# Optimization experiments

Measured on AMD Instinct MI355X. Metric: run time of the kernel, lower is better.

The kernel has to match this reference:

```python
import jax, jax.numpy as jnp
import numpy as np

PS = 16          # patch size == conv kernel == stride
EPS = 1e-5       # BatchNorm eps (torch default)


def setup_inputs() -> dict:
    key = jax.random.key(0)
    ks = jax.random.split(key, 12)
    B, Cin, H = 64, 3, 256
    D, Dm = 3, 768                      # private_depth, hidden_dim
    P = (H // PS) ** 2                  # num_patches = 256

    x = jax.random.normal(ks[0], (B, Cin, H, H), jnp.float32)
    # patch-embed conv: weight [O, I, kh, kw], bias [O]
    conv0_w = jax.random.normal(ks[1], (Dm, Cin, PS, PS), jnp.float32) * 0.02
    conv0_b = jax.random.normal(ks[2], (Dm,), jnp.float32) * 0.02
    # depth x (1x1 conv + BN): stacked params
    w1 = jax.random.normal(ks[3], (D, Dm, Dm), jnp.float32) * 0.02   # [O, I]
    b1 = jax.random.normal(ks[4], (D, Dm), jnp.float32) * 0.02
    gamma = jnp.ones((D, Dm), jnp.float32)
    beta = jnp.zeros((D, Dm), jnp.float32)
    # positional embedding [1, P, Dm]
    pos_emb = jax.random.normal(ks[5], (1, P, Dm), jnp.float32)
    # mixer Linear [out, in] + bias
    mixer_w = jax.random.normal(ks[6], (Dm, Dm), jnp.float32) * 0.02
    mixer_b = jax.random.normal(ks[7], (Dm,), jnp.float32) * 0.02
    # per-sample random permutation of the P patches (replaces randperm loop)
    perm = jax.vmap(lambda k: jax.random.permutation(k, P))(
        jax.random.split(ks[8], B)).astype(jnp.int32)

    return {"x": x, "conv0_w": conv0_w, "conv0_b": conv0_b, "w1": w1,
            "b1": b1, "gamma": gamma, "beta": beta, "pos_emb": pos_emb,
            "mixer_w": mixer_w, "mixer_b": mixer_b, "perm": perm}


def reference(x, conv0_w, conv0_b, w1, b1, gamma, beta, pos_emb,
              mixer_w, mixer_b, perm):
    B, Cin, H, W = x.shape
    hp, wp = H // PS, W // PS
    Dm = conv0_w.shape[0]

    # non-overlapping patch conv == reshape + matmul
    # x -> [B, hp*wp, Cin*PS*PS] with (c, kh, kw) flattening matching conv weight
    patches = x.reshape(B, Cin, hp, PS, wp, PS).transpose(0, 2, 4, 1, 3, 5)
    patches = patches.reshape(B, hp * wp, Cin * PS * PS)
    h = jax.nn.relu(patches @ conv0_w.reshape(Dm, -1).T + conv0_b)  # [B, P, Dm]

    # private_depth x (1x1 conv -> BN (batch stats, no running stats) -> ReLU)
    for d in range(w1.shape[0]):
        h = h @ w1[d].T + b1[d]
        mu = h.mean(axis=(0, 1))                      # per-channel over (B, H*W)
        var = ((h - mu) ** 2).mean(axis=(0, 1))       # biased variance
        h = (h - mu) * jax.lax.rsqrt(var + EPS) * gamma[d] + beta[d]
        h = jax.nn.relu(h)

    # pos embedding + mixer (ReLU -> Linear)
    h = h + pos_emb
    h = jax.nn.relu(h) @ mixer_w.T + mixer_b          # [B, P, Dm]

    # per-sample pixel shuffle: shuffled[i, j] = h[i, perm[i, j]]
    out = jnp.take_along_axis(h, perm[:, :, None].astype(jnp.int32), axis=1)
    return out
```

## Files before the change

kernel.cpp:

```cpp
#include <hip/hip_runtime.h>
#include <hip/hip_bf16.h>
#include <stdint.h>

#define M_TOT 16384
#define DM 768
#define BM 256
#define BN 192
#define NKT3 12
#define QOFF (128 * DM)

typedef __attribute__((ext_vector_type(4))) float f32x4;
typedef __attribute__((ext_vector_type(8))) short short8;
typedef __attribute__((ext_vector_type(8))) unsigned short ushort8;
typedef __attribute__((ext_vector_type(4))) unsigned short ushort4v;

__device__ __forceinline__ unsigned short f2bf(float f) {
    union { float f; unsigned u; } v; v.f = f;
    unsigned r = v.u + 0x7fffu + ((v.u >> 16) & 1u);
    return (unsigned short)(r >> 16);
}
__device__ __forceinline__ float bf2f(unsigned short h) {
    union { unsigned u; float f; } v; v.u = ((unsigned)h) << 16;
    return v.f;
}

__device__ __forceinline__ void gload_lds16(const unsigned short* g, unsigned short* l) {
    __builtin_amdgcn_global_load_lds(
        (const __attribute__((address_space(1))) void*)g,
        (__attribute__((address_space(3))) void*)l, 16, 0, 0);
}

__global__ __launch_bounds__(256)
void prepim(const float* __restrict__ cw, const float* __restrict__ w1,
            const float* __restrict__ mw, const int* __restrict__ perm,
            const float* __restrict__ x,
            unsigned short* __restrict__ wA, unsigned short* __restrict__ wD,
            unsigned short* __restrict__ wM, int* __restrict__ invp,
            unsigned short* __restrict__ patches)
{
    int b = blockIdx.x;
    if (b < 12288) {
        int t = b * 256 + threadIdx.x;
        int bp = t / 192;
        int q  = t - bp * 192;
        int c   = q >> 6;
        int kh  = (q >> 2) & 15;
        int kw0 = (q & 3) << 2;
        int bb = bp >> 8, p = bp & 255;
        int ph = p >> 4, pw = p & 15;
        const float* src = x + ((((size_t)bb * 3 + c) * 256 + ph * 16 + kh) * 256 + pw * 16 + kw0);
        f32x4 v = *(const f32x4*)src;
        ushort4v o;
        o.x = f2bf(v.x); o.y = f2bf(v.y); o.z = f2bf(v.z); o.w = f2bf(v.w);
        *(ushort4v*)(patches + (size_t)bp * DM + (q << 2)) = o;
    } else if (b < 12288 + 2880) {
        int i = (b - 12288) * 256 + threadIdx.x;
        const float* src; unsigned short* dst; int off;
        if (i < 147456)              { src = cw; dst = wA; off = i; }
        else if (i < 147456+442368)  { src = w1; dst = wD; off = i - 147456; }
        else                         { src = mw; dst = wM; off = i - 589824; }
        f32x4 v = ((const f32x4*)src)[off];
        ushort4v o;
        o.x = f2bf(v.x); o.y = f2bf(v.y); o.z = f2bf(v.z); o.w = f2bf(v.w);
        ((ushort4v*)dst)[off] = o;
    } else {
        int i = (b - 12288 - 2880) * 256 + threadIdx.x;
        int bb = i >> 8;
        invp[(bb << 8) + perm[i]] = i & 255;
    }
}

#define VM4  asm volatile("s_waitcnt vmcnt(4)" ::: "memory");
#define VM0  asm volatile("s_waitcnt vmcnt(0)" ::: "memory");
#define LGKM0 asm volatile("s_waitcnt lgkmcnt(0)" ::: "memory");
#define BARR asm volatile("s_barrier" ::: "memory");

#define PH(AB, BB, MH, KS, LOADB, PRE, POST)                                     \
  {                                                                              \
    if (LOADB) {                                                                 \
      _Pragma("unroll")                                                          \
      for (int j = 0; j < 3; ++j)                                                \
        breg[j] = *(const short8*)((const char*)Bb + (size_t)(BB) * (BN*64*2) +  \
                  (wc * 48 + j * 16 + frow) * 128 + (((KS) * 64 + fq16) ^ rswz));\
    }                                                                            \
    short8 af[4];                                                                \
    _Pragma("unroll")                                                            \
    for (int i = 0; i < 4; ++i)                                                  \
      af[i] = *(const short8*)((const char*)Aa + (size_t)(AB) * (BM*64*2) +      \
              (wr * 128 + (MH) * 64 + i * 16 + frow) * 128 +                     \
              (((KS) * 64 + fq16) ^ rswz));                                      \
    PRE;                                                                         \
    __builtin_amdgcn_s_setprio(1);                                               \
    _Pragma("unroll")                                                            \
    for (int i = 0; i < 4; ++i)                                                  \
      _Pragma("unroll")                                                          \
      for (int j = 0; j < 3; ++j)                                                \
        acc[(MH) * 4 + i][j] = __builtin_amdgcn_mfma_f32_16x16x32_bf16(          \
            af[i], breg[j], acc[(MH) * 4 + i][j], 0, 0, 0);                      \
    __builtin_amdgcn_s_setprio(0);                                               \
    POST;                                                                        \
    BARR                                                                         \
  }

template<int EPI, int BNA>
__global__ __launch_bounds__(512, 2)
void gemm8p(const unsigned short* __restrict__ A,
            const unsigned short* __restrict__ Bw,
            const float* __restrict__ bias,
            void* __restrict__ outp,
            const int* __restrict__ invp,
            float* __restrict__ bnpart,
            const float* __restrict__ ssA)
{
    __shared__ unsigned short Aa[3][BM * 64];
    __shared__ unsigned short Bb[2][BN * 64];

    const int tid  = threadIdx.x;
    const int w    = tid >> 6;
    const int lane = tid & 63;
    const int wr = w >> 2, wc = w & 3;

    int bid = blockIdx.x;
    int nb  = (bid & 7) * 32 + (bid >> 3);
    const int tileM = nb >> 2, tileN = nb & 3;
    const int m0 = tileM * BM, n0 = tileN * BN;

    const int sRow = lane >> 3;
    const int swzc = ((lane & 7) * 16) ^ ((sRow & 7) << 4);
    const unsigned short* gA0 = A  + (size_t)(m0 + w * 32 + sRow) * DM + (swzc >> 1);
    const unsigned short* gB0 = Bw + (size_t)(n0 + w * 24 + sRow) * DM + (swzc >> 1);

    auto STAGE_A = [&](int buf, int kt) {
        #pragma unroll
        for (int j = 0; j < 4; ++j)
            gload_lds16(gA0 + (size_t)j * 8 * DM + kt * 64,
                        &Aa[buf][(w * 32 + j * 8) * 64]);
    };
    auto STAGE_B = [&](int buf, int kt) {
        #pragma unroll
        for (int j = 0; j < 3; ++j)
            gload_lds16(gB0 + (size_t)j * 8 * DM + kt * 64,
                        &Bb[buf][(w * 24 + j * 8) * 64]);
    };

    const int rRow0 = w * 32 + (lane >> 3);
    const unsigned short* gAr = A + (size_t)(m0 + rRow0) * DM + (lane & 7) * 8;
    const int wrswz = (lane >> 3) << 4;
    ushort8 aldr[4];

    auto ALOAD = [&](int t) {
        #pragma unroll
        for (int j = 0; j < 4; ++j)
            aldr[j] = *(const ushort8*)(gAr + (size_t)j * 8 * DM + t * 64);
    };
    auto XFORM = [&](int t, int tb) {
        const int k0 = t * 64 + (lane & 7) * 8;
        f32x4 sa = *(const f32x4*)(ssA + k0);
        f32x4 sb = *(const f32x4*)(ssA + k0 + 4);
        f32x4 ha = *(const f32x4*)(ssA + DM + k0);
        f32x4 hb = *(const f32x4*)(ssA + DM + k0 + 4);
        #pragma unroll
        for (int j = 0; j < 4; ++j) {
            int row = rRow0 + j * 8;
            ushort8 u = aldr[j];
            ushort8 o;
            #pragma unroll
            for (int e = 0; e < 8; ++e) {
                float f = bf2f(u[e]);
                float sc = (e < 4) ? sa[e] : sb[e - 4];
                float sh = (e < 4) ? ha[e] : hb[e - 4];
                o[e] = f2bf(fmaxf(fmaf(sc, f, sh), 0.0f));
            }
            *(ushort8*)((char*)Aa + (size_t)tb * (BM*64*2) + row * 128 +
                        (((lane & 7) * 16) ^ wrswz)) = o;
        }
    };

    const int frow = lane & 15;
    const int fq16 = (lane >> 4) * 16;
    const int rswz = (lane & 7) << 4;

    f32x4 acc[8][3] = {};
    short8 breg[3];

    if (BNA == 0) {
        STAGE_A(0, 0);
        STAGE_B(0, 0);
        STAGE_A(1, 1);
        VM4
        BARR
    } else {
        ALOAD(0); XFORM(0, 0);
        ALOAD(1); XFORM(1, 1);
        STAGE_B(0, 0);
        VM0
        LGKM0
        BARR
    }

    if (BNA == 0) {
        #pragma unroll
        for (int kt = 0; kt < NKT3; ++kt) {
            const int ab = kt % 3, bb = kt & 1;
            PH(ab, bb, 0, 0, 1, { if (kt < 11) STAGE_B((kt + 1) & 1, kt + 1); }, {})
            PH(ab, bb, 1, 0, 0, { if (kt < 10) STAGE_A((kt + 2) % 3, kt + 2); }, {})
            PH(ab, bb, 0, 1, 1, {}, {})
            if (kt < 10)       { PH(ab, bb, 1, 1, 0, {}, { VM4 }) }
            else if (kt == 10) { PH(ab, bb, 1, 1, 0, {}, { VM0 }) }
            else               { PH(ab, bb, 1, 1, 0, {}, {}) }
        }
    } else {
        #pragma unroll 3
        for (int kt = 0; kt < NKT3; ++kt) {
            const int ab = kt % 3, bb = kt & 1;
            const int ab1 = (ab == 2) ? 0 : ab + 1;
            PH(ab, bb, 0, 0, 1, { if (kt < 11) STAGE_B((kt + 1) & 1, kt + 1); }, {})
            PH(ab, bb, 1, 0, 0, { if (kt >= 1 && kt < 11) XFORM(kt + 1, ab1); },
                                { if (kt >= 1 && kt < 11) LGKM0 })
            PH(ab, bb, 0, 1, 1, {}, {})
            PH(ab, bb, 1, 1, 0, {}, { if (kt < 11) VM0
                                      if (kt < 10) ALOAD(kt + 2); })
        }
    }

    const int crow = (lane >> 4) * 4;
    const int ccol = lane & 15;
    const int nbase = n0 + wc * 48;

    float bv[3];
    #pragma unroll
    for (int j = 0; j < 3; ++j) bv[j] = bias[nbase + j * 16 + ccol];

    if (EPI == 0) {
        unsigned short* O = (unsigned short*)outp;
        #pragma unroll
        for (int mi = 0; mi < 8; ++mi) {
            #pragma unroll
            for (int r = 0; r < 4; ++r) {
                int m = m0 + wr * 128 + mi * 16 + crow + r;
                unsigned short* orow = O + (size_t)m * DM + nbase + ccol;
                #pragma unroll
                for (int j = 0; j < 3; ++j)
                    orow[j * 16] = f2bf(fmaxf(acc[mi][j][r] + bv[j], 0.0f));
            }
        }
    }

    if (EPI == 2) {
        float* O = (float*)outp;
        #pragma unroll
        for (int mi = 0; mi < 8; ++mi) {
            #pragma unroll
            for (int r = 0; r < 4; ++r) {
                int m = m0 + wr * 128 + mi * 16 + crow + r;
                int mo = (m & ~255) | invp[m];
                float* orow = O + (size_t)mo * DM + nbase + ccol;
                #pragma unroll
                for (int j = 0; j < 3; ++j)
                    orow[j * 16] = acc[mi][j][r] + bv[j];
            }
        }
    }

    if (EPI == 1) {
        unsigned short* O = (unsigned short*)outp;
        #pragma unroll
        for (int mi = 0; mi < 8; ++mi) {
            #pragma unroll
            for (int r = 0; r < 4; ++r) {
                int m = m0 + wr * 128 + mi * 16 + crow + r;
                unsigned short* orow = O + (size_t)m * DM + nbase + ccol;
                #pragma unroll
                for (int j = 0; j < 3; ++j)
                    orow[j * 16] = f2bf(acc[mi][j][r] + bv[j]);
            }
        }
        #pragma unroll
        for (int j = 0; j < 3; ++j) {
            float s = 0.f, q = 0.f;
            #pragma unroll
            for (int mi = 0; mi < 8; ++mi)
                #pragma unroll
                for (int r = 0; r < 4; ++r) {
                    float v = acc[mi][j][r] + bv[j];
                    s += v; q += v * v;
                }
            s += __shfl_xor(s, 16); s += __shfl_xor(s, 32);
            q += __shfl_xor(q, 16); q += __shfl_xor(q, 32);
            if (lane < 16) {
                int c  = nbase + j * 16 + lane;
                int ri = tileM * 2 + wr;
                bnpart[(size_t)c * 128 + ri]        = s;
                bnpart[QOFF + (size_t)c * 128 + ri] = q;
            }
        }
    }
}

__global__ void bn_stats(const float* __restrict__ part, const float* __restrict__ gamma,
                         const float* __restrict__ beta, float* __restrict__ ss)
{
    int c = blockIdx.x * 256 + threadIdx.x;
    const float* ps = part + (size_t)c * 128;
    const float* pq = part + QOFF + (size_t)c * 128;
    float s = 0.f, q = 0.f;
    #pragma unroll 8
    for (int i = 0; i < 128; ++i) { s += ps[i]; q += pq[i]; }
    float mu  = s * (1.0f / 16384.0f);
    float var = q * (1.0f / 16384.0f) - mu * mu;
    float scale = rsqrtf(var + 1e-5f) * gamma[c];
    ss[c] = scale;
    ss[DM + c] = beta[c] - mu * scale;
}

__global__ __launch_bounds__(256)
void bnpos_apply(const unsigned short* __restrict__ hin, const float* __restrict__ ss,
                 const float* __restrict__ pos, unsigned short* __restrict__ hout)
{
    __shared__ float sc[DM], sh[DM];
    const int t = threadIdx.x;
    #pragma unroll
    for (int i = 0; i < 3; ++i) {
        sc[t + i * 256] = ss[t + i * 256];
        sh[t + i * 256] = ss[DM + t + i * 256];
    }
    __syncthreads();

    int g = blockIdx.x * 256 + t;
    int row = g / 96;
    int c0 = (g - row * 96) * 8;
    const short8 v = *(const short8*)(hin + (size_t)row * DM + c0);
    short8 o;
    #pragma unroll
    for (int e = 0; e < 8; ++e) {
        float xv = bf2f((unsigned short)v[e]);
        float y = fmaxf(xv * sc[c0 + e] + sh[c0 + e], 0.0f);
        y = fmaxf(y + pos[(row & 255) * DM + c0 + e], 0.0f);
        o[e] = (short)f2bf(y);
    }
    *(short8*)(hout + (size_t)row * DM + c0) = o;
}

extern "C" void kernel_launch(void* const* d_in, const int* in_sizes, int n_in,
                              void* d_out, int out_size, void* d_ws, size_t ws_size,
                              hipStream_t stream)
{
    (void)in_sizes; (void)n_in; (void)out_size; (void)ws_size;

    const float* x       = (const float*)d_in[0];
    const float* conv0_w = (const float*)d_in[1];
    const float* conv0_b = (const float*)d_in[2];
    const float* w1      = (const float*)d_in[3];
    const float* b1      = (const float*)d_in[4];
    const float* gamma   = (const float*)d_in[5];
    const float* beta    = (const float*)d_in[6];
    const float* pos     = (const float*)d_in[7];
    const float* mixer_w = (const float*)d_in[8];
    const float* mixer_b = (const float*)d_in[9];
    const int*   perm    = (const int*)d_in[10];

    unsigned short* actA = (unsigned short*)d_ws;
    unsigned short* actB = actA + (size_t)M_TOT * DM;
    unsigned short* wA   = actB + (size_t)M_TOT * DM;
    unsigned short* wD   = wA + DM * DM;
    unsigned short* wM   = wD + 3 * DM * DM;
    float* bnpart = (float*)(wM + DM * DM);
    float* ss     = bnpart + 2 * 128 * DM;
    int*   invp   = (int*)(ss + 2 * DM);

    prepim<<<15232, 256, 0, stream>>>(conv0_w, w1, mixer_w, perm, x,
                                      wA, wD, wM, invp, actA);

    gemm8p<0, 0><<<256, 512, 0, stream>>>(actA, wA, conv0_b, actB, nullptr,
                                          nullptr, nullptr);
    gemm8p<1, 0><<<256, 512, 0, stream>>>(actB, wD + 0 * (size_t)DM * DM, b1 + 0 * DM,
                                          actA, nullptr, bnpart, nullptr);
    bn_stats<<<3, 256, 0, stream>>>(bnpart, gamma + 0 * DM, beta + 0 * DM, ss);
    gemm8p<1, 1><<<256, 512, 0, stream>>>(actA, wD + 1 * (size_t)DM * DM, b1 + 1 * DM,
                                          actB, nullptr, bnpart, ss);
    bn_stats<<<3, 256, 0, stream>>>(bnpart, gamma + 1 * DM, beta + 1 * DM, ss);
    gemm8p<1, 1><<<256, 512, 0, stream>>>(actB, wD + 2 * (size_t)DM * DM, b1 + 2 * DM,
                                          actA, nullptr, bnpart, ss);
    bn_stats<<<3, 256, 0, stream>>>(bnpart, gamma + 2 * DM, beta + 2 * DM, ss);
    bnpos_apply<<<6144, 256, 0, stream>>>(actA, ss, pos, actB);
    gemm8p<2, 0><<<256, 512, 0, stream>>>(actB, wM, mixer_b, d_out, invp,
                                          nullptr, nullptr);
}
```

Before: 207.4 us.

## Switch GEMM to 32x32x16 MFMA with 4x2 wave layout

Replaces the 16x16x32 bf16 MFMA tiling with 32x32x16 MFMAs, reorganising the 8 waves from a 2x4 to a 4x2 grid so each wave computes 64x96 instead of 128x48. Fragment loads from LDS shrink per FLOP, and the main loop is restructured into two half-k phases per tile instead of four. The epilogue indexing and the BN partial-sum layout change accordingly (256 row partials per channel instead of 128), which doubles the work in bn_stats. It risks register pressure and different LDS bank behaviour with the larger accumulator tiles.

```diff
diff --git a/kernel.cpp b/kernel.cpp
--- a/kernel.cpp
+++ b/kernel.cpp
@@ -7,9 +7,10 @@
 #define BM 256
 #define BN 192
 #define NKT3 12
-#define QOFF (128 * DM)
+#define QOFF (256 * DM)
 
 typedef __attribute__((ext_vector_type(4))) float f32x4;
+typedef __attribute__((ext_vector_type(16))) float f32x16;
 typedef __attribute__((ext_vector_type(8))) short short8;
 typedef __attribute__((ext_vector_type(8))) unsigned short ushort8;
 typedef __attribute__((ext_vector_type(4))) unsigned short ushort4v;
@@ -75,32 +76,32 @@
 #define LGKM0 asm volatile("s_waitcnt lgkmcnt(0)" ::: "memory");
 #define BARR asm volatile("s_barrier" ::: "memory");
 
-#define PH(AB, BB, MH, KS, LOADB, PRE, POST)                                     \
-  {                                                                              \
-    if (LOADB) {                                                                 \
+#define FRAGS(AB, BB, H)                                                         \
+    short8 af[2][2], br[3][2];                                                   \
+    _Pragma("unroll")                                                            \
+    for (int s = 0; s < 2; ++s) {                                                \
+      const int kb = ((2*(H)+s) * 32 + khalf) ^ rswz;                            \
       _Pragma("unroll")                                                          \
-      for (int j = 0; j < 3; ++j)                                                \
-        breg[j] = *(const short8*)((const char*)Bb + (size_t)(BB) * (BN*64*2) +  \
-                  (wc * 48 + j * 16 + frow) * 128 + (((KS) * 64 + fq16) ^ rswz));\
-    }                                                                            \
-    short8 af[4];                                                                \
-    _Pragma("unroll")                                                            \
-    for (int i = 0; i < 4; ++i)                                                  \
-      af[i] = *(const short8*)((const char*)Aa + (size_t)(AB) * (BM*64*2) +      \
-              (wr * 128 + (MH) * 64 + i * 16 + frow) * 128 +                     \
-              (((KS) * 64 + fq16) ^ rswz));                                      \
-    PRE;                                                                         \
+      for (int mi = 0; mi < 2; ++mi)                                             \
+        af[mi][s] = *(const short8*)((const char*)Aa + (size_t)(AB)*(BM*64*2) +  \
+                    (wr*64 + mi*32 + cl)*128 + kb);                              \
+      _Pragma("unroll")                                                          \
+      for (int nj = 0; nj < 3; ++nj)                                             \
+        br[nj][s] = *(const short8*)((const char*)Bb + (size_t)(BB)*(BN*64*2) +  \
+                    (wc*96 + nj*32 + cl)*128 + kb);                              \
+    }
+
+#define MFMAS                                                                    \
     __builtin_amdgcn_s_setprio(1);                                               \
     _Pragma("unroll")                                                            \
-    for (int i = 0; i < 4; ++i)                                                  \
+    for (int s = 0; s < 2; ++s)                                                  \
       _Pragma("unroll")                                                          \
-      for (int j = 0; j < 3; ++j)                                                \
-        acc[(MH) * 4 + i][j] = __builtin_amdgcn_mfma_f32_16x16x32_bf16(          \
-            af[i], breg[j], acc[(MH) * 4 + i][j], 0, 0, 0);                      \
-    __builtin_amdgcn_s_setprio(0);                                               \
-    POST;                                                                        \
-    BARR                                                                         \
-  }
+      for (int mi = 0; mi < 2; ++mi)                                             \
+        _Pragma("unroll")                                                        \
+        for (int nj = 0; nj < 3; ++nj)                                           \
+          acc[mi][nj] = __builtin_amdgcn_mfma_f32_32x32x16_bf16(                 \
+              af[mi][s], br[nj][s], acc[mi][nj], 0, 0, 0);                       \
+    __builtin_amdgcn_s_setprio(0);
 
 template<int EPI, int BNA>
 __global__ __launch_bounds__(512, 2)
@@ -118,7 +119,7 @@
     const int tid  = threadIdx.x;
     const int w    = tid >> 6;
     const int lane = tid & 63;
-    const int wr = w >> 2, wc = w & 3;
+    const int wr = w >> 1, wc = w & 1;
 
     int bid = blockIdx.x;
     int nb  = (bid & 7) * 32 + (bid >> 3);
@@ -176,12 +177,11 @@
         }
     };
 
-    const int frow = lane & 15;
-    const int fq16 = (lane >> 4) * 16;
+    const int cl = lane & 31;
+    const int khalf = (lane >> 5) * 16;
     const int rswz = (lane & 7) << 4;
 
-    f32x4 acc[8][3] = {};
-    short8 breg[3];
+    f32x16 acc[2][3] = {};
 
     if (BNA == 0) {
         STAGE_A(0, 0);
@@ -202,46 +202,54 @@
         #pragma unroll
         for (int kt = 0; kt < NKT3; ++kt) {
             const int ab = kt % 3, bb = kt & 1;
-            PH(ab, bb, 0, 0, 1, { if (kt < 11) STAGE_B((kt + 1) & 1, kt + 1); }, {})
-            PH(ab, bb, 1, 0, 0, { if (kt < 10) STAGE_A((kt + 2) % 3, kt + 2); }, {})
-            PH(ab, bb, 0, 1, 1, {}, {})
-            if (kt < 10)       { PH(ab, bb, 1, 1, 0, {}, { VM4 }) }
-            else if (kt == 10) { PH(ab, bb, 1, 1, 0, {}, { VM0 }) }
-            else               { PH(ab, bb, 1, 1, 0, {}, {}) }
+            { FRAGS(ab, bb, 0)
+              if (kt < 11) STAGE_B((kt + 1) & 1, kt + 1);
+              MFMAS
+              BARR }
+            { FRAGS(ab, bb, 1)
+              if (kt < 10) STAGE_A((kt + 2) % 3, kt + 2);
+              MFMAS
+              if (kt < 10)       { VM4 }
+              else if (kt == 10) { VM0 }
+              BARR }
         }
     } else {
         #pragma unroll 3
         for (int kt = 0; kt < NKT3; ++kt) {
             const int ab = kt % 3, bb = kt & 1;
             const int ab1 = (ab == 2) ? 0 : ab + 1;
-            PH(ab, bb, 0, 0, 1, { if (kt < 11) STAGE_B((kt + 1) & 1, kt + 1); }, {})
-            PH(ab, bb, 1, 0, 0, { if (kt >= 1 && kt < 11) XFORM(kt + 1, ab1); },
-                                { if (kt >= 1 && kt < 11) LGKM0 })
-            PH(ab, bb, 0, 1, 1, {}, {})
-            PH(ab, bb, 1, 1, 0, {}, { if (kt < 11) VM0
-                                      if (kt < 10) ALOAD(kt + 2); })
-        }
-    }
-
-    const int crow = (lane >> 4) * 4;
-    const int ccol = lane & 15;
-    const int nbase = n0 + wc * 48;
+            { FRAGS(ab, bb, 0)
+              if (kt < 11) STAGE_B((kt + 1) & 1, kt + 1);
+              MFMAS
+              BARR }
+            { FRAGS(ab, bb, 1)
+              if (kt >= 1 && kt < 11) XFORM(kt + 1, ab1);
+              MFMAS
+              if (kt >= 1 && kt < 11) { LGKM0 }
+              if (kt < 11) { VM0 }
+              if (kt < 10) ALOAD(kt + 2);
+              BARR }
+        }
+    }
+
+    const int rhi = (lane >> 5) * 4;
+    const int nbase = n0 + wc * 96;
 
     float bv[3];
     #pragma unroll
-    for (int j = 0; j < 3; ++j) bv[j] = bias[nbase + j * 16 + ccol];
+    for (int nj = 0; nj < 3; ++nj) bv[nj] = bias[nbase + nj * 32 + cl];
 
     if (EPI == 0) {
         unsigned short* O = (unsigned short*)outp;
         #pragma unroll
-        for (int mi = 0; mi < 8; ++mi) {
-            #pragma unroll
-            for (int r = 0; r < 4; ++r) {
-                int m = m0 + wr * 128 + mi * 16 + crow + r;
-                unsigned short* orow = O + (size_t)m * DM + nbase + ccol;
+        for (int mi = 0; mi < 2; ++mi) {
+            #pragma unroll
+            for (int r = 0; r < 16; ++r) {
+                int m = m0 + wr * 64 + mi * 32 + (r & 3) + 8 * (r >> 2) + rhi;
+                unsigned short* orow = O + (size_t)m * DM + nbase + cl;
                 #pragma unroll
-                for (int j = 0; j < 3; ++j)
-                    orow[j * 16] = f2bf(fmaxf(acc[mi][j][r] + bv[j], 0.0f));
+                for (int nj = 0; nj < 3; ++nj)
+                    orow[nj * 32] = f2bf(fmaxf(acc[mi][nj][r] + bv[nj], 0.0f));
             }
         }
     }
@@ -249,15 +257,15 @@
     if (EPI == 2) {
         float* O = (float*)outp;
         #pragma unroll
-        for (int mi = 0; mi < 8; ++mi) {
-            #pragma unroll
-            for (int r = 0; r < 4; ++r) {
-                int m = m0 + wr * 128 + mi * 16 + crow + r;
+        for (int mi = 0; mi < 2; ++mi) {
+            #pragma unroll
+            for (int r = 0; r < 16; ++r) {
+                int m = m0 + wr * 64 + mi * 32 + (r & 3) + 8 * (r >> 2) + rhi;
                 int mo = (m & ~255) | invp[m];
-                float* orow = O + (size_t)mo * DM + nbase + ccol;
+                float* orow = O + (size_t)mo * DM + nbase + cl;
                 #pragma unroll
-                for (int j = 0; j < 3; ++j)
-                    orow[j * 16] = acc[mi][j][r] + bv[j];
+                for (int nj = 0; nj < 3; ++nj)
+                    orow[nj * 32] = acc[mi][nj][r] + bv[nj];
             }
         }
     }
@@ -265,33 +273,33 @@
     if (EPI == 1) {
         unsigned short* O = (unsigned short*)outp;
         #pragma unroll
-        for (int mi = 0; mi < 8; ++mi) {
-            #pragma unroll
-            for (int r = 0; r < 4; ++r) {
-                int m = m0 + wr * 128 + mi * 16 + crow + r;
-                unsigned short* orow = O + (size_t)m * DM + nbase + ccol;
+        for (int mi = 0; mi < 2; ++mi) {
+            #pragma unroll
+            for (int r = 0; r < 16; ++r) {
+                int m = m0 + wr * 64 + mi * 32 + (r & 3) + 8 * (r >> 2) + rhi;
+                unsigned short* orow = O + (size_t)m * DM + nbase + cl;
                 #pragma unroll
-                for (int j = 0; j < 3; ++j)
-                    orow[j * 16] = f2bf(acc[mi][j][r] + bv[j]);
-            }
-        }
-        #pragma unroll
-        for (int j = 0; j < 3; ++j) {
+                for (int nj = 0; nj < 3; ++nj)
+                    orow[nj * 32] = f2bf(acc[mi][nj][r] + bv[nj]);
+            }
+        }
+        #pragma unroll
+        for (int nj = 0; nj < 3; ++nj) {
             float s = 0.f, q = 0.f;
             #pragma unroll
-            for (int mi = 0; mi < 8; ++mi)
+            for (int mi = 0; mi < 2; ++mi)
                 #pragma unroll
-                for (int r = 0; r < 4; ++r) {
-                    float v = acc[mi][j][r] + bv[j];
+                for (int r = 0; r < 16; ++r) {
+                    float v = acc[mi][nj][r] + bv[nj];
                     s += v; q += v * v;
                 }
-            s += __shfl_xor(s, 16); s += __shfl_xor(s, 32);
-            q += __shfl_xor(q, 16); q += __shfl_xor(q, 32);
-            if (lane < 16) {
-                int c  = nbase + j * 16 + lane;
-                int ri = tileM * 2 + wr;
-                bnpart[(size_t)c * 128 + ri]        = s;
-                bnpart[QOFF + (size_t)c * 128 + ri] = q;
+            s += __shfl_xor(s, 32);
+            q += __shfl_xor(q, 32);
+            if (lane < 32) {
+                int c  = nbase + nj * 32 + cl;
+                int ri = tileM * 4 + wr;
+                bnpart[(size_t)c * 256 + ri]        = s;
+                bnpart[QOFF + (size_t)c * 256 + ri] = q;
             }
         }
     }
@@ -301,11 +309,11 @@
                          const float* __restrict__ beta, float* __restrict__ ss)
 {
     int c = blockIdx.x * 256 + threadIdx.x;
-    const float* ps = part + (size_t)c * 128;
-    const float* pq = part + QOFF + (size_t)c * 128;
+    const float* ps = part + (size_t)c * 256;
+    const float* pq = part + QOFF + (size_t)c * 256;
     float s = 0.f, q = 0.f;
     #pragma unroll 8
-    for (int i = 0; i < 128; ++i) { s += ps[i]; q += pq[i]; }
+    for (int i = 0; i < 256; ++i) { s += ps[i]; q += pq[i]; }
     float mu  = s * (1.0f / 16384.0f);
     float var = q * (1.0f / 16384.0f) - mu * mu;
     float scale = rsqrtf(var + 1e-5f) * gamma[c];
@@ -365,7 +373,7 @@
     unsigned short* wD   = wA + DM * DM;
     unsigned short* wM   = wD + 3 * DM * DM;
     float* bnpart = (float*)(wM + DM * DM);
-    float* ss     = bnpart + 2 * 128 * DM;
+    float* ss     = bnpart + 2 * 256 * DM;
     int*   invp   = (int*)(ss + 2 * DM);
 
     prepim<<<15232, 256, 0, stream>>>(conv0_w, w1, mixer_w, perm, x,
```

After: 227.8 us. 9.8% more time.

## Halve GEMM M-tile to 128 with 4-wave blocks and double-buffered A

Applied to the files above, without the earlier changes.

Each GEMM block now covers 128 rows instead of 256 and runs four waves instead of eight, so each launch has twice as many blocks. The A shared-memory ring drops from a triple buffer to a double buffer. The prefetch distance falls to one k-tile, with a full vmcnt(0) wait every iteration. BN partial-sum indexing changes to one slot per M-tile. The smaller tile spreads work over more CUs but raises B-operand reload traffic and exposes more load latency.

```diff
diff --git a/kernel.cpp b/kernel.cpp
--- a/kernel.cpp
+++ b/kernel.cpp
@@ -4,7 +4,7 @@
 
 #define M_TOT 16384
 #define DM 768
-#define BM 256
+#define BM 128
 #define BN 192
 #define NKT3 12
 #define QOFF (128 * DM)
@@ -70,7 +70,6 @@
     }
 }
 
-#define VM4  asm volatile("s_waitcnt vmcnt(4)" ::: "memory");
 #define VM0  asm volatile("s_waitcnt vmcnt(0)" ::: "memory");
 #define LGKM0 asm volatile("s_waitcnt lgkmcnt(0)" ::: "memory");
 #define BARR asm volatile("s_barrier" ::: "memory");
@@ -87,7 +86,7 @@
     _Pragma("unroll")                                                            \
     for (int i = 0; i < 4; ++i)                                                  \
       af[i] = *(const short8*)((const char*)Aa + (size_t)(AB) * (BM*64*2) +      \
-              (wr * 128 + (MH) * 64 + i * 16 + frow) * 128 +                     \
+              ((MH) * 64 + i * 16 + frow) * 128 +                                \
               (((KS) * 64 + fq16) ^ rswz));                                      \
     PRE;                                                                         \
     __builtin_amdgcn_s_setprio(1);                                               \
@@ -103,7 +102,7 @@
   }
 
 template<int EPI, int BNA>
-__global__ __launch_bounds__(512, 2)
+__global__ __launch_bounds__(256, 2)
 void gemm8p(const unsigned short* __restrict__ A,
             const unsigned short* __restrict__ Bw,
             const float* __restrict__ bias,
@@ -112,23 +111,23 @@
             float* __restrict__ bnpart,
             const float* __restrict__ ssA)
 {
-    __shared__ unsigned short Aa[3][BM * 64];
+    __shared__ unsigned short Aa[2][BM * 64];
     __shared__ unsigned short Bb[2][BN * 64];
 
     const int tid  = threadIdx.x;
     const int w    = tid >> 6;
     const int lane = tid & 63;
-    const int wr = w >> 2, wc = w & 3;
+    const int wc = w;
 
     int bid = blockIdx.x;
-    int nb  = (bid & 7) * 32 + (bid >> 3);
+    int nb  = (bid & 7) * 64 + (bid >> 3);
     const int tileM = nb >> 2, tileN = nb & 3;
     const int m0 = tileM * BM, n0 = tileN * BN;
 
     const int sRow = lane >> 3;
     const int swzc = ((lane & 7) * 16) ^ ((sRow & 7) << 4);
     const unsigned short* gA0 = A  + (size_t)(m0 + w * 32 + sRow) * DM + (swzc >> 1);
-    const unsigned short* gB0 = Bw + (size_t)(n0 + w * 24 + sRow) * DM + (swzc >> 1);
+    const unsigned short* gB0 = Bw + (size_t)(n0 + w * 48 + sRow) * DM + (swzc >> 1);
 
     auto STAGE_A = [&](int buf, int kt) {
         #pragma unroll
@@ -138,9 +137,9 @@
     };
     auto STAGE_B = [&](int buf, int kt) {
         #pragma unroll
-        for (int j = 0; j < 3; ++j)
+        for (int j = 0; j < 6; ++j)
             gload_lds16(gB0 + (size_t)j * 8 * DM + kt * 64,
-                        &Bb[buf][(w * 24 + j * 8) * 64]);
+                        &Bb[buf][(w * 48 + j * 8) * 64]);
     };
 
     const int rRow0 = w * 32 + (lane >> 3);
@@ -186,12 +185,11 @@
     if (BNA == 0) {
         STAGE_A(0, 0);
         STAGE_B(0, 0);
-        STAGE_A(1, 1);
-        VM4
+        VM0
         BARR
     } else {
         ALOAD(0); XFORM(0, 0);
-        ALOAD(1); XFORM(1, 1);
+        ALOAD(1);
         STAGE_B(0, 0);
         VM0
         LGKM0
@@ -201,25 +199,24 @@
     if (BNA == 0) {
         #pragma unroll
         for (int kt = 0; kt < NKT3; ++kt) {
-            const int ab = kt % 3, bb = kt & 1;
-            PH(ab, bb, 0, 0, 1, { if (kt < 11) STAGE_B((kt + 1) & 1, kt + 1); }, {})
-            PH(ab, bb, 1, 0, 0, { if (kt < 10) STAGE_A((kt + 2) % 3, kt + 2); }, {})
-            PH(ab, bb, 0, 1, 1, {}, {})
-            if (kt < 10)       { PH(ab, bb, 1, 1, 0, {}, { VM4 }) }
-            else if (kt == 10) { PH(ab, bb, 1, 1, 0, {}, { VM0 }) }
-            else               { PH(ab, bb, 1, 1, 0, {}, {}) }
+            const int cb = kt & 1, nbuf = cb ^ 1;
+            PH(cb, cb, 0, 0, 1, { if (kt < 11) STAGE_B(nbuf, kt + 1); }, {})
+            PH(cb, cb, 1, 0, 0, { if (kt < 11) STAGE_A(nbuf, kt + 1); }, {})
+            PH(cb, cb, 0, 1, 1, {}, {})
+            if (kt < 11) { PH(cb, cb, 1, 1, 0, {}, { VM0 }) }
+            else         { PH(cb, cb, 1, 1, 0, {}, {}) }
         }
     } else {
-        #pragma unroll 3
+        #pragma unroll 2
         for (int kt = 0; kt < NKT3; ++kt) {
-            const int ab = kt % 3, bb = kt & 1;
-            const int ab1 = (ab == 2) ? 0 : ab + 1;
-            PH(ab, bb, 0, 0, 1, { if (kt < 11) STAGE_B((kt + 1) & 1, kt + 1); }, {})
-            PH(ab, bb, 1, 0, 0, { if (kt >= 1 && kt < 11) XFORM(kt + 1, ab1); },
-                                { if (kt >= 1 && kt < 11) LGKM0 })
-            PH(ab, bb, 0, 1, 1, {}, {})
-            PH(ab, bb, 1, 1, 0, {}, { if (kt < 11) VM0
-                                      if (kt < 10) ALOAD(kt + 2); })
+            const int cb = kt & 1, nbuf = cb ^ 1;
+            PH(cb, cb, 0, 0, 1, { if (kt < 11) STAGE_B(nbuf, kt + 1); }, {})
+            PH(cb, cb, 1, 0, 0, { if (kt < 11) XFORM(kt + 1, nbuf); },
+                                { if (kt < 11) LGKM0 })
+            PH(cb, cb, 0, 1, 1, {}, {})
+            if (kt < 11) { PH(cb, cb, 1, 1, 0, {}, { VM0
+                                                     if (kt < 10) ALOAD(kt + 2); }) }
+            else         { PH(cb, cb, 1, 1, 0, {}, {}) }
         }
     }
 
@@ -237,7 +234,7 @@
         for (int mi = 0; mi < 8; ++mi) {
             #pragma unroll
             for (int r = 0; r < 4; ++r) {
-                int m = m0 + wr * 128 + mi * 16 + crow + r;
+                int m = m0 + mi * 16 + crow + r;
                 unsigned short* orow = O + (size_t)m * DM + nbase + ccol;
                 #pragma unroll
                 for (int j = 0; j < 3; ++j)
@@ -252,7 +249,7 @@
         for (int mi = 0; mi < 8; ++mi) {
             #pragma unroll
             for (int r = 0; r < 4; ++r) {
-                int m = m0 + wr * 128 + mi * 16 + crow + r;
+                int m = m0 + mi * 16 + crow + r;
                 int mo = (m & ~255) | invp[m];
                 float* orow = O + (size_t)mo * DM + nbase + ccol;
                 #pragma unroll
@@ -268,7 +265,7 @@
         for (int mi = 0; mi < 8; ++mi) {
             #pragma unroll
             for (int r = 0; r < 4; ++r) {
-                int m = m0 + wr * 128 + mi * 16 + crow + r;
+                int m = m0 + mi * 16 + crow + r;
                 unsigned short* orow = O + (size_t)m * DM + nbase + ccol;
                 #pragma unroll
                 for (int j = 0; j < 3; ++j)
@@ -288,10 +285,9 @@
             s += __shfl_xor(s, 16); s += __shfl_xor(s, 32);
             q += __shfl_xor(q, 16); q += __shfl_xor(q, 32);
             if (lane < 16) {
-                int c  = nbase + j * 16 + lane;
-                int ri = tileM * 2 + wr;
-                bnpart[(size_t)c * 128 + ri]        = s;
-                bnpart[QOFF + (size_t)c * 128 + ri] = q;
+                int c = nbase + j * 16 + lane;
+                bnpart[(size_t)c * 128 + tileM]        = s;
+                bnpart[QOFF + (size_t)c * 128 + tileM] = q;
             }
         }
     }
@@ -371,18 +367,18 @@
     prepim<<<15232, 256, 0, stream>>>(conv0_w, w1, mixer_w, perm, x,
                                       wA, wD, wM, invp, actA);
 
-    gemm8p<0, 0><<<256, 512, 0, stream>>>(actA, wA, conv0_b, actB, nullptr,
+    gemm8p<0, 0><<<512, 256, 0, stream>>>(actA, wA, conv0_b, actB, nullptr,
                                           nullptr, nullptr);
-    gemm8p<1, 0><<<256, 512, 0, stream>>>(actB, wD + 0 * (size_t)DM * DM, b1 + 0 * DM,
+    gemm8p<1, 0><<<512, 256, 0, stream>>>(actB, wD + 0 * (size_t)DM * DM, b1 + 0 * DM,
                                           actA, nullptr, bnpart, nullptr);
     bn_stats<<<3, 256, 0, stream>>>(bnpart, gamma + 0 * DM, beta + 0 * DM, ss);
-    gemm8p<1, 1><<<256, 512, 0, stream>>>(actA, wD + 1 * (size_t)DM * DM, b1 + 1 * DM,
+    gemm8p<1, 1><<<512, 256, 0, stream>>>(actA, wD + 1 * (size_t)DM * DM, b1 + 1 * DM,
                                           actB, nullptr, bnpart, ss);
     bn_stats<<<3, 256, 0, stream>>>(bnpart, gamma + 1 * DM, beta + 1 * DM, ss);
-    gemm8p<1, 1><<<256, 512, 0, stream>>>(actB, wD + 2 * (size_t)DM * DM, b1 + 2 * DM,
+    gemm8p<1, 1><<<512, 256, 0, stream>>>(actB, wD + 2 * (size_t)DM * DM, b1 + 2 * DM,
                                           actA, nullptr, bnpart, ss);
     bn_stats<<<3, 256, 0, stream>>>(bnpart, gamma + 2 * DM, beta + 2 * DM, ss);
     bnpos_apply<<<6144, 256, 0, stream>>>(actA, ss, pos, actB);
-    gemm8p<2, 0><<<256, 512, 0, stream>>>(actB, wM, mixer_b, d_out, invp,
+    gemm8p<2, 0><<<512, 256, 0, stream>>>(actB, wM, mixer_b, d_out, invp,
                                           nullptr, nullptr);
 }
```

New measurement: 198.1 us. 1.05x faster.
